# Performance work log

Hardware: AMD Instinct MI355X
Metric: run time of the kernel (lower is better)

Reference implementation:

```python
import jax, jax.numpy as jnp
import numpy as np

SCALE = 2
STRIDE = 1


def setup_inputs() -> dict:
    key = jax.random.key(0)
    kx, kw, kb = jax.random.split(key, 3)
    B, Cin, H, W = 16, 128, 64, 64
    Cout, kh, kw_ = 128, 3, 3
    N = Cout * Cin * kh * kw_
    bound = 1.0 / np.sqrt(N)
    x = jax.random.normal(kx, (B, Cin, H, W), dtype=jnp.float32)
    weight = jax.random.uniform(kw, (Cout, Cin, kh, kw_), dtype=jnp.float32,
                                minval=-bound, maxval=bound)
    bias = jax.random.uniform(kb, (Cout,), dtype=jnp.float32,
                              minval=-bound, maxval=bound)
    return {"x": x, "weight": weight, "bias": bias}


def reference(x, weight, bias):
    # Nearest-neighbor upsample: each input pixel replicated SCALE x SCALE.
    up = jnp.repeat(jnp.repeat(x, SCALE, axis=2), SCALE, axis=3)  # [B,C,H*s,W*s]
    # Conv2d (cross-correlation, no padding), same math as unfold + matmul.
    out = jax.lax.conv_general_dilated(
        up, weight,
        window_strides=(STRIDE, STRIDE),
        padding="VALID",
        dimension_numbers=("NCHW", "OIHW", "NCHW"),
    )
    return out + bias[None, :, None, None]
```

## Files before the change

### kernel.cpp

```cpp
#include <hip/hip_runtime.h>
#include <hip/hip_bf16.h>
#include <stdint.h>


#define B_    16
#define CIN   128
#define HIN   64
#define WIN   64
#define COUT  128
#define HO    126
#define WO    126
#define M_TOT (B_ * 63 * 63)
#define BM    64
#define KTILES 16
#define AS_K  520

typedef __bf16 bf16;
typedef __bf16 bf16x4 __attribute__((ext_vector_type(4)));
typedef __bf16 bf16x8 __attribute__((ext_vector_type(8)));
typedef float  floatx4 __attribute__((ext_vector_type(4)));

__global__ void prep_weights(const float* __restrict__ w, bf16* __restrict__ wb) {
    int idx = blockIdx.x * 256 + threadIdx.x;
    if (idx >= 4 * KTILES * COUT * 32) return;
    int k32 = idx & 31;
    int o   = (idx >> 5) & 127;
    int par = (idx >> 12) & 3;
    int kt  = idx >> 14;
    int k = kt * 32 + k32;
    int c = k >> 2, u = (k >> 1) & 1, v = k & 1;
    int a = par >> 1, bp = par & 1;
    int dy0, dy1, ndy, dx0, dx1, ndx;
    if (u == 0) { if (a == 0) { dy0 = 0; dy1 = 1; ndy = 2; } else { dy0 = 0; dy1 = 0; ndy = 1; } }
    else        { if (a == 0) { dy0 = 2; dy1 = 2; ndy = 1; } else { dy0 = 1; dy1 = 2; ndy = 2; } }
    if (v == 0) { if (bp == 0) { dx0 = 0; dx1 = 1; ndx = 2; } else { dx0 = 0; dx1 = 0; ndx = 1; } }
    else        { if (bp == 0) { dx0 = 2; dx1 = 2; ndx = 1; } else { dx0 = 1; dx1 = 2; ndx = 2; } }
    const float* wp = w + (o * CIN + c) * 9;
    float s = wp[dy0 * 3 + dx0];
    if (ndx == 2) s += wp[dy0 * 3 + dx1];
    if (ndy == 2) { s += wp[dy1 * 3 + dx0]; if (ndx == 2) s += wp[dy1 * 3 + dx1]; }
    wb[idx] = (bf16)s;
}

__global__ __launch_bounds__(512, 4)
void upconv_gemm(const float* __restrict__ x, const bf16* __restrict__ wb,
                 const float* __restrict__ bias, float* __restrict__ out) {
    __shared__ bf16 As[BM * AS_K];

    const int t    = threadIdx.x;
    const int lane = t & 63;
    const int wid  = t >> 6;
    const int a    = wid >> 2;
    const int oq   = wid & 3;
    const int quad = lane >> 4;
    const int l15  = lane & 15;
    const int kq   = quad * 8;

    const int m0 = blockIdx.x * BM;

    const int ml = lane;
    const int m_mine = m0 + ml;
    const bool mvalid = (m_mine < M_TOT);
    int b_ = 0, p_ = 0, q_ = 0;
    if (mvalid) { b_ = m_mine / 3969; int rr = m_mine - b_ * 3969; p_ = rr / 63; q_ = rr - p_ * 63; }
    const float* xbase = x + ((size_t)(b_ * CIN) * HIN + p_) * WIN + q_;

    #pragma unroll
    for (int cc = 0; cc < 16; ++cc) {
        const int c = wid * 16 + cc;
        float f00 = 0.f, f01 = 0.f, f10 = 0.f, f11 = 0.f;
        if (mvalid) {
            const float* pa = xbase + (size_t)c * (HIN * WIN);
            f00 = pa[0]; f01 = pa[1]; f10 = pa[WIN]; f11 = pa[WIN + 1];
        }
        bf16x4 v; v[0] = (bf16)f00; v[1] = (bf16)f01; v[2] = (bf16)f10; v[3] = (bf16)f11;
        *(bf16x4*)&As[ml * AS_K + c * 4] = v;
    }
    __syncthreads();

    const bf16* wwave = wb + ((size_t)(a * 2) * COUT + oq * 32 + l15) * 32 + kq;

    floatx4 acc[2][4][2] = {};

    #pragma unroll
    for (int kt = 0; kt < KTILES; ++kt) {
        bf16x8 af[4], wf[2][2];
        #pragma unroll
        for (int i = 0; i < 4; ++i)
            af[i] = *(const bf16x8*)&As[(i * 16 + l15) * AS_K + kt * 32 + kq];
        #pragma unroll
        for (int bp = 0; bp < 2; ++bp)
            #pragma unroll
            for (int nt = 0; nt < 2; ++nt)
                wf[bp][nt] = *(const bf16x8*)(wwave
                    + ((size_t)kt * 4 * COUT + (size_t)bp * COUT + nt * 16) * 32);
        #pragma unroll
        for (int bp = 0; bp < 2; ++bp)
            #pragma unroll
            for (int mt = 0; mt < 4; ++mt)
                #pragma unroll
                for (int nt = 0; nt < 2; ++nt)
                    acc[bp][mt][nt] = __builtin_amdgcn_mfma_f32_16x16x32_bf16(
                        wf[bp][nt], af[mt], acc[bp][mt][nt], 0, 0, 0);
    }

    float bv[2][4];
    #pragma unroll
    for (int nt = 0; nt < 2; ++nt)
        #pragma unroll
        for (int ri = 0; ri < 4; ++ri)
            bv[nt][ri] = bias[oq * 32 + nt * 16 + quad * 4 + ri];

    #pragma unroll
    for (int mt = 0; mt < 4; ++mt) {
        const int m = m0 + mt * 16 + l15;
        const bool v = (m < M_TOT);
        int b = 0, p = 0, q = 0;
        if (v) { b = m / 3969; int rr = m - b * 3969; p = rr / 63; q = rr - p * 63; }
        float* base = out + (size_t)b * (COUT * HO * WO) + (size_t)(2 * p + a) * WO + 2 * q;
        #pragma unroll
        for (int nt = 0; nt < 2; ++nt) {
            #pragma unroll
            for (int ri = 0; ri < 4; ++ri) {
                const int o = oq * 32 + nt * 16 + quad * 4 + ri;
                if (v) {
                    float2 r = make_float2(acc[0][mt][nt][ri] + bv[nt][ri],
                                           acc[1][mt][nt][ri] + bv[nt][ri]);
                    *(float2*)(base + (size_t)o * (HO * WO)) = r;
                }
            }
        }
    }
}

extern "C" void kernel_launch(void* const* d_in, const int* in_sizes, int n_in,
                              void* d_out, int out_size, void* d_ws, size_t ws_size,
                              hipStream_t stream) {
    const float* x    = (const float*)d_in[0];
    const float* w    = (const float*)d_in[1];
    const float* bias = (const float*)d_in[2];
    float* out = (float*)d_out;
    bf16* wb = (bf16*)d_ws;

    prep_weights<<<(4 * KTILES * COUT * 32 + 255) / 256, 256, 0, stream>>>(w, wb);

    dim3 grid((M_TOT + BM - 1) / BM);
    upconv_gemm<<<grid, 512, 0, stream>>>(x, wb, bias, out);
}
```

Baseline: 216.3 us.

## Double-buffer MFMA operand fragments and prefetch first weight tiles before staging

Restructures the K loop to hold two sets of A and weight fragments, loading the next tile pair while MFMAs on the current one run. Wave priority is raised around the MFMA blocks. The first weight loads are issued before the shared-memory staging so their latency overlaps it. The launch-bounds occupancy hint drops from 4 to 2 to make room for the extra registers, which may reduce the number of resident waves.

```diff
diff --git a/kernel.cpp b/kernel.cpp
--- a/kernel.cpp
+++ b/kernel.cpp
@@ -42,7 +42,7 @@
     wb[idx] = (bf16)s;
 }
 
-__global__ __launch_bounds__(512, 4)
+__global__ __launch_bounds__(512, 2)
 void upconv_gemm(const float* __restrict__ x, const bf16* __restrict__ wb,
                  const float* __restrict__ bias, float* __restrict__ out) {
     __shared__ bf16 As[BM * AS_K];
@@ -57,6 +57,19 @@
     const int kq   = quad * 8;
 
     const int m0 = blockIdx.x * BM;
+
+    const bf16* wwave = wb + ((size_t)(a * 2) * COUT + oq * 32 + l15) * 32 + kq;
+
+    bf16x8 wfA[2][2], wfB[2][2];
+    #pragma unroll
+    for (int bp = 0; bp < 2; ++bp)
+        #pragma unroll
+        for (int nt = 0; nt < 2; ++nt) {
+            wfA[bp][nt] = *(const bf16x8*)(wwave
+                + ((size_t)0 * 4 * COUT + (size_t)bp * COUT + nt * 16) * 32);
+            wfB[bp][nt] = *(const bf16x8*)(wwave
+                + ((size_t)1 * 4 * COUT + (size_t)bp * COUT + nt * 16) * 32);
+        }
 
     const int ml = lane;
     const int m_mine = m0 + ml;
@@ -78,22 +91,18 @@
     }
     __syncthreads();
 
-    const bf16* wwave = wb + ((size_t)(a * 2) * COUT + oq * 32 + l15) * 32 + kq;
+    bf16x8 afA[4], afB[4];
+    #pragma unroll
+    for (int i = 0; i < 4; ++i) {
+        afA[i] = *(const bf16x8*)&As[(i * 16 + l15) * AS_K + 0 * 32 + kq];
+        afB[i] = *(const bf16x8*)&As[(i * 16 + l15) * AS_K + 1 * 32 + kq];
+    }
 
     floatx4 acc[2][4][2] = {};
 
     #pragma unroll
-    for (int kt = 0; kt < KTILES; ++kt) {
-        bf16x8 af[4], wf[2][2];
-        #pragma unroll
-        for (int i = 0; i < 4; ++i)
-            af[i] = *(const bf16x8*)&As[(i * 16 + l15) * AS_K + kt * 32 + kq];
-        #pragma unroll
-        for (int bp = 0; bp < 2; ++bp)
-            #pragma unroll
-            for (int nt = 0; nt < 2; ++nt)
-                wf[bp][nt] = *(const bf16x8*)(wwave
-                    + ((size_t)kt * 4 * COUT + (size_t)bp * COUT + nt * 16) * 32);
+    for (int kt2 = 0; kt2 < KTILES; kt2 += 2) {
+        __builtin_amdgcn_s_setprio(1);
         #pragma unroll
         for (int bp = 0; bp < 2; ++bp)
             #pragma unroll
@@ -101,7 +110,45 @@
                 #pragma unroll
                 for (int nt = 0; nt < 2; ++nt)
                     acc[bp][mt][nt] = __builtin_amdgcn_mfma_f32_16x16x32_bf16(
-                        wf[bp][nt], af[mt], acc[bp][mt][nt], 0, 0, 0);
+                        wfA[bp][nt], afA[mt], acc[bp][mt][nt], 0, 0, 0);
+        __builtin_amdgcn_s_setprio(0);
+
+        if (kt2 + 2 < KTILES) {
+            const int ktn = kt2 + 2;
+            #pragma unroll
+            for (int i = 0; i < 4; ++i)
+                afA[i] = *(const bf16x8*)&As[(i * 16 + l15) * AS_K + ktn * 32 + kq];
+            #pragma unroll
+            for (int bp = 0; bp < 2; ++bp)
+                #pragma unroll
+                for (int nt = 0; nt < 2; ++nt)
+                    wfA[bp][nt] = *(const bf16x8*)(wwave
+                        + ((size_t)ktn * 4 * COUT + (size_t)bp * COUT + nt * 16) * 32);
+        }
+
+        __builtin_amdgcn_s_setprio(1);
+        #pragma unroll
+        for (int bp = 0; bp < 2; ++bp)
+            #pragma unroll
+            for (int mt = 0; mt < 4; ++mt)
+                #pragma unroll
+                for (int nt = 0; nt < 2; ++nt)
+                    acc[bp][mt][nt] = __builtin_amdgcn_mfma_f32_16x16x32_bf16(
+                        wfB[bp][nt], afB[mt], acc[bp][mt][nt], 0, 0, 0);
+        __builtin_amdgcn_s_setprio(0);
+
+        if (kt2 + 3 < KTILES) {
+            const int ktn = kt2 + 3;
+            #pragma unroll
+            for (int i = 0; i < 4; ++i)
+                afB[i] = *(const bf16x8*)&As[(i * 16 + l15) * AS_K + ktn * 32 + kq];
+            #pragma unroll
+            for (int bp = 0; bp < 2; ++bp)
+                #pragma unroll
+                for (int nt = 0; nt < 2; ++nt)
+                    wfB[bp][nt] = *(const bf16x8*)(wwave
+                        + ((size_t)ktn * 4 * COUT + (size_t)bp * COUT + nt * 16) * 32);
+        }
     }
 
     float bv[2][4];
```

New measurement: 233.3 us. 7.9% more time.

## Swizzle LDS A-tile and stage output through LDS for coalesced stores

Applied to the files above, without the earlier changes.

The A tile is now written to LDS as 8-element bf16 vectors, pairing two channels, with an XOR swizzle on the 8-element group index, and MFMA operand reads use the matching swizzle to reduce bank conflicts. The epilogue writes accumulators into LDS (reusing the A buffer) and then has each wave write contiguous output rows, so global stores run along q rather than being scattered by the MFMA output layout. Index arithmetic also drops size_t casts to 32-bit. In exchange this adds extra barriers, an LDS round-trip of the accumulators and a partly serialized epilogue over the two output-row parities.

```diff
diff --git a/kernel.cpp b/kernel.cpp
--- a/kernel.cpp
+++ b/kernel.cpp
@@ -16,7 +16,6 @@
 #define AS_K  520
 
 typedef __bf16 bf16;
-typedef __bf16 bf16x4 __attribute__((ext_vector_type(4)));
 typedef __bf16 bf16x8 __attribute__((ext_vector_type(8)));
 typedef float  floatx4 __attribute__((ext_vector_type(4)));
 
@@ -46,6 +45,7 @@
 void upconv_gemm(const float* __restrict__ x, const bf16* __restrict__ wb,
                  const float* __restrict__ bias, float* __restrict__ out) {
     __shared__ bf16 As[BM * AS_K];
+    float* Ld = reinterpret_cast<float*>(As);
 
     const int t    = threadIdx.x;
     const int lane = t & 63;
@@ -58,27 +58,35 @@
 
     const int m0 = blockIdx.x * BM;
 
-    const int ml = lane;
-    const int m_mine = m0 + ml;
-    const bool mvalid = (m_mine < M_TOT);
-    int b_ = 0, p_ = 0, q_ = 0;
-    if (mvalid) { b_ = m_mine / 3969; int rr = m_mine - b_ * 3969; p_ = rr / 63; q_ = rr - p_ * 63; }
-    const float* xbase = x + ((size_t)(b_ * CIN) * HIN + p_) * WIN + q_;
+    {
+        const int ml = lane;
+        const int m_mine = m0 + ml;
+        const bool mvalid = (m_mine < M_TOT);
+        int b_ = 0, p_ = 0, q_ = 0;
+        if (mvalid) { b_ = m_mine / 3969; int rr = m_mine - b_ * 3969; p_ = rr / 63; q_ = rr - p_ * 63; }
+        const float* xbase = x + ((b_ * CIN) * HIN + p_) * WIN + q_;
+        const int xsw = ml & 7;
 
-    #pragma unroll
-    for (int cc = 0; cc < 16; ++cc) {
-        const int c = wid * 16 + cc;
-        float f00 = 0.f, f01 = 0.f, f10 = 0.f, f11 = 0.f;
-        if (mvalid) {
-            const float* pa = xbase + (size_t)c * (HIN * WIN);
-            f00 = pa[0]; f01 = pa[1]; f10 = pa[WIN]; f11 = pa[WIN + 1];
+        #pragma unroll
+        for (int j = 0; j < 8; ++j) {
+            const int c0 = wid * 16 + 2 * j;
+            float f0[4] = {0.f, 0.f, 0.f, 0.f}, f1[4] = {0.f, 0.f, 0.f, 0.f};
+            if (mvalid) {
+                const float* pa = xbase + c0 * (HIN * WIN);
+                f0[0] = pa[0]; f0[1] = pa[1]; f0[2] = pa[WIN]; f0[3] = pa[WIN + 1];
+                const float* pb = pa + (HIN * WIN);
+                f1[0] = pb[0]; f1[1] = pb[1]; f1[2] = pb[WIN]; f1[3] = pb[WIN + 1];
+            }
+            bf16x8 v;
+            v[0] = (bf16)f0[0]; v[1] = (bf16)f0[1]; v[2] = (bf16)f0[2]; v[3] = (bf16)f0[3];
+            v[4] = (bf16)f1[0]; v[5] = (bf16)f1[1]; v[6] = (bf16)f1[2]; v[7] = (bf16)f1[3];
+            const int g = wid * 8 + j;
+            *(bf16x8*)&As[ml * AS_K + ((g ^ xsw) * 8)] = v;
         }
-        bf16x4 v; v[0] = (bf16)f00; v[1] = (bf16)f01; v[2] = (bf16)f10; v[3] = (bf16)f11;
-        *(bf16x4*)&As[ml * AS_K + c * 4] = v;
     }
     __syncthreads();
 
-    const bf16* wwave = wb + ((size_t)(a * 2) * COUT + oq * 32 + l15) * 32 + kq;
+    const bf16* wwave = wb + ((a * 2) * COUT + oq * 32 + l15) * 32 + kq;
 
     floatx4 acc[2][4][2] = {};
 
@@ -86,14 +94,16 @@
     for (int kt = 0; kt < KTILES; ++kt) {
         bf16x8 af[4], wf[2][2];
         #pragma unroll
-        for (int i = 0; i < 4; ++i)
-            af[i] = *(const bf16x8*)&As[(i * 16 + l15) * AS_K + kt * 32 + kq];
+        for (int i = 0; i < 4; ++i) {
+            const int row = i * 16 + l15;
+            af[i] = *(const bf16x8*)&As[row * AS_K + (((kt * 4 + quad) ^ (row & 7)) * 8)];
+        }
         #pragma unroll
         for (int bp = 0; bp < 2; ++bp)
             #pragma unroll
             for (int nt = 0; nt < 2; ++nt)
                 wf[bp][nt] = *(const bf16x8*)(wwave
-                    + ((size_t)kt * 4 * COUT + (size_t)bp * COUT + nt * 16) * 32);
+                    + (kt * 4 * COUT + bp * COUT + nt * 16) * 32);
         #pragma unroll
         for (int bp = 0; bp < 2; ++bp)
             #pragma unroll
@@ -104,30 +114,50 @@
                         wf[bp][nt], af[mt], acc[bp][mt][nt], 0, 0, 0);
     }
 
-    float bv[2][4];
-    #pragma unroll
-    for (int nt = 0; nt < 2; ++nt)
-        #pragma unroll
-        for (int ri = 0; ri < 4; ++ri)
-            bv[nt][ri] = bias[oq * 32 + nt * 16 + quad * 4 + ri];
+    const int b_base = m0 / 3969;
+    const int rr0 = m0 - b_base * 3969;
+    const int p0  = rr0 / 63;
+    const int q   = lane;
 
     #pragma unroll
-    for (int mt = 0; mt < 4; ++mt) {
-        const int m = m0 + mt * 16 + l15;
-        const bool v = (m < M_TOT);
-        int b = 0, p = 0, q = 0;
-        if (v) { b = m / 3969; int rr = m - b * 3969; p = rr / 63; q = rr - p * 63; }
-        float* base = out + (size_t)b * (COUT * HO * WO) + (size_t)(2 * p + a) * WO + 2 * q;
-        #pragma unroll
-        for (int nt = 0; nt < 2; ++nt) {
+    for (int ap = 0; ap < 2; ++ap) {
+        __syncthreads();
+
+        if (a == ap) {
             #pragma unroll
-            for (int ri = 0; ri < 4; ++ri) {
-                const int o = oq * 32 + nt * 16 + quad * 4 + ri;
-                if (v) {
-                    float2 r = make_float2(acc[0][mt][nt][ri] + bv[nt][ri],
-                                           acc[1][mt][nt][ri] + bv[nt][ri]);
-                    *(float2*)(base + (size_t)o * (HO * WO)) = r;
-                }
+            for (int bp = 0; bp < 2; ++bp)
+                #pragma unroll
+                for (int mt = 0; mt < 4; ++mt)
+                    #pragma unroll
+                    for (int nt = 0; nt < 2; ++nt)
+                        #pragma unroll
+                        for (int ri = 0; ri < 4; ++ri) {
+                            const int o   = oq * 32 + nt * 16 + quad * 4 + ri;
+                            const int mlx = (mt * 16 + l15) ^ (quad << 4);
+                            Ld[(o * 2 + bp) * 64 + mlx] = acc[bp][mt][nt][ri];
+                        }
+        }
+        __syncthreads();
+
+        for (int i = 0; i < 32; ++i) {
+            const int rid = wid * 32 + i;
+            const int o   = rid >> 1;
+            const int pi  = rid & 1;
+            int b = b_base, p = p0 + pi;
+            if (p > 62) { b += 1; p = 0; }
+            if (b >= B_) continue;
+            const int base_m = b * 3969 + p * 63;
+            const float bo = bias[o];
+            const int m_lane = base_m + q;
+            const bool val = (q < 63) && (m_lane >= m0) && (m_lane < m0 + BM) && (m_lane < M_TOT);
+            if (val) {
+                const int mloc = m_lane - m0;
+                const int xsw  = ((o >> 2) & 3) << 4;
+                const float v0 = Ld[(o * 2 + 0) * 64 + (mloc ^ xsw)];
+                const float v1 = Ld[(o * 2 + 1) * 64 + (mloc ^ xsw)];
+                const int y = 2 * p + ap;
+                float* dst = out + b * (COUT * HO * WO) + o * (HO * WO) + y * WO + 2 * q;
+                *(float2*)dst = make_float2(v0 + bo, v1 + bo);
             }
         }
     }
```

New measurement: 214.1 us. No clear change (-1.0%).
